# Performance work log

Measured on AMD Instinct MI355X. Metric: run time of the kernel, lower is better.

## Reference

```python
import jax, jax.numpy as jnp
import numpy as np

B, NV, CIN, C = 1, 40000, 128, 64
D, H, W = 19, 200, 176  # sparse_shape = output_shape[1:4] + [1,0,0]
EPS = 1e-3
DN = ('NCDHW', 'OIDHW', 'NCDHW')


def setup_inputs():
    key = jax.random.key(0)
    ks = jax.random.split(key, 12)
    vf = jax.random.normal(ks[0], (NV, CIN), jnp.float32)
    bi = jnp.zeros((NV, 1), jnp.int32)
    zi = jax.random.randint(ks[1], (NV, 1), 0, D, jnp.int32)
    yi = jax.random.randint(ks[2], (NV, 1), 0, H, jnp.int32)
    xi = jax.random.randint(ks[3], (NV, 1), 0, W, jnp.int32)
    coors = jnp.concatenate([bi, zi, yi, xi], axis=1)  # [batch, z, y, x]
    s = 0.05
    w_sub1 = jax.random.normal(ks[4], (C, CIN, 3, 3, 3), jnp.float32) * s
    w_down1 = jax.random.normal(ks[5], (C, C, 3, 1, 1), jnp.float32) * s
    w_sub2 = jax.random.normal(ks[6], (C, C, 3, 3, 3), jnp.float32) * s
    w_sub3 = jax.random.normal(ks[7], (C, C, 3, 3, 3), jnp.float32) * s
    w_down2 = jax.random.normal(ks[8], (C, C, 3, 1, 1), jnp.float32) * s
    bn_gamma = 1.0 + 0.1 * jax.random.normal(ks[9], (5, C), jnp.float32)
    bn_beta = 0.1 * jax.random.normal(ks[10], (5, C), jnp.float32)
    bn_mean = 0.1 * jax.random.normal(ks[11], (5, C), jnp.float32)
    bn_var = jnp.ones((5, C), jnp.float32)
    return dict(voxel_features=vf, coors=coors, batch_size=1,
                w_sub1=w_sub1, w_down1=w_down1, w_sub2=w_sub2, w_sub3=w_sub3,
                w_down2=w_down2, bn_gamma=bn_gamma, bn_beta=bn_beta,
                bn_mean=bn_mean, bn_var=bn_var)


def _conv(x, w, stride, pad):
    return jax.lax.conv_general_dilated(x, w, stride, pad, dimension_numbers=DN)


def _bnrelu(x, i, mask, g, b, m, v):
    # eval-mode BN on active sites only (inactive sites stay exactly zero -> mask)
    inv = jax.lax.rsqrt(v[i] + EPS)
    y = (x - m[i][None, :, None, None, None]) * (g[i] * inv)[None, :, None, None, None] \
        + b[i][None, :, None, None, None]
    return jnp.maximum(y, 0.0) * mask


def _forward(voxel_features, coors, batch_size, w_sub1, w_down1, w_sub2, w_sub3,
             w_down2, bn_gamma, bn_beta, bn_mean, bn_var):
    bi, zi, yi, xi = coors[:, 0], coors[:, 1], coors[:, 2], coors[:, 3]
    # scn.InputLayer: scatter (sum duplicates) active voxel features into dense grid
    dense = jnp.zeros((batch_size, D, H, W, CIN), voxel_features.dtype)
    dense = dense.at[bi, zi, yi, xi].add(voxel_features)
    x = jnp.transpose(dense, (0, 4, 1, 2, 3))  # NCDHW
    mask = jnp.zeros((batch_size, D, H, W), voxel_features.dtype)
    mask = mask.at[bi, zi, yi, xi].set(1.0)[:, None]  # [B,1,D,H,W] active sites
    ones_k = jnp.ones((1, 1, 3, 1, 1), x.dtype)
    pad1 = ((1, 1), (1, 1), (1, 1))
    bn = (bn_gamma, bn_beta, bn_mean, bn_var)
    # SubmanifoldConvolution(128->64, k3) + BNReLU : output only at active sites
    x = _bnrelu(_conv(x, w_sub1, (1, 1, 1), pad1) * mask, 0, mask, *bn)
    # Convolution 64->64 kernel (3,1,1) stride (2,1,1): new active set = any input in window
    x = _conv(x, w_down1, (2, 1, 1), 'VALID')
    mask = (_conv(mask, ones_k, (2, 1, 1), 'VALID') > 0).astype(x.dtype)
    x = _bnrelu(x, 1, mask, *bn)
    # two more submanifold convs
    x = _bnrelu(_conv(x, w_sub2, (1, 1, 1), pad1) * mask, 2, mask, *bn)
    x = _bnrelu(_conv(x, w_sub3, (1, 1, 1), pad1) * mask, 3, mask, *bn)
    # second strided conv
    x = _conv(x, w_down2, (2, 1, 1), 'VALID')
    mask = (_conv(mask, ones_k, (2, 1, 1), 'VALID') > 0).astype(x.dtype)
    x = _bnrelu(x, 4, mask, *bn)
    # SparseToDense then view(N, C*D, H, W)
    Nb, Cc, Dd, Hh, Ww = x.shape
    return x.reshape(Nb, Cc * Dd, Hh, Ww)


def reference(voxel_features, coors, batch_size, w_sub1, w_down1, w_sub2, w_sub3,
              w_down2, bn_gamma, bn_beta, bn_mean, bn_var):
    return _forward(voxel_features, coors, batch_size, w_sub1, w_down1, w_sub2,
                    w_sub3, w_down2, bn_gamma, bn_beta, bn_mean, bn_var)
```

## Files before the change

kernel.cpp:

```cpp
#include <hip/hip_runtime.h>

typedef float floatx4 __attribute__((ext_vector_type(4)));
typedef __bf16 bf16x8 __attribute__((ext_vector_type(8)));

#define D0_ 19
#define H0_ 200
#define W0_ 176
#define HW_ (H0_*W0_)
#define NCELL0 (D0_*HW_)
#define D1_ 9
#define NCELL1 (D1_*HW_)
#define D2_ 4
#define NCELL2 (D2_*HW_)
#define NV_ 40000
#define CAP0 40000
#define CAP1 80000
#define CAP2 140800
#define EPS_ 1e-3f

typedef __attribute__((address_space(1))) const unsigned int* gas_t;
typedef __attribute__((address_space(3))) unsigned int* las_t;

__device__ __forceinline__ float bf2f(short s){
    union { unsigned u; float f; } x; x.u = ((unsigned)(unsigned short)s) << 16; return x.f;
}
__device__ __forceinline__ short f2bf(float f){
    union { float f; unsigned u; } x; x.f = f;
    unsigned r = x.u + 0x7fffu + ((x.u >> 16) & 1u);
    return (short)(r >> 16);
}

__device__ __forceinline__ void repack_one(const float* w, short* Bout, int i, int KCsrc, int NSP){
    int k = i >> 6, n = i & 63;
    int ci = k & 127;
    int cis = (KCsrc == 128) ? ci : (ci & 63);
    short val = f2bf(w[(n * KCsrc + cis) * NSP + (k >> 7)]);
    int kc = k >> 5, lanehi = (k >> 3) & 3, jj = k & 7;
    int nt = n >> 4, lane = lanehi * 16 + (n & 15);
    Bout[((kc * 4 + nt) * 64 + lane) * 8 + jj] = val;
}

#define RP_BIG (3456*64)
#define RP_SML (384*64)

__global__ void k_prep(const float* w1, const float* w2, const float* w3,
                       const float* wd1, const float* wd2,
                       short* B1, short* B2, short* B3, short* Bd1, short* Bd2,
                       const float* g, const float* b, const float* m, const float* v,
                       float* scale, float* shift){
    int i = blockIdx.x * 256 + threadIdx.x;
    if (i < RP_BIG){ repack_one(w1, B1, i, 128, 27); return; }
    i -= RP_BIG;
    if (i < RP_BIG){ repack_one(w2, B2, i, 64, 27); return; }
    i -= RP_BIG;
    if (i < RP_BIG){ repack_one(w3, B3, i, 64, 27); return; }
    i -= RP_BIG;
    if (i < RP_SML){ repack_one(wd1, Bd1, i, 64, 3); return; }
    i -= RP_SML;
    if (i < RP_SML){ repack_one(wd2, Bd2, i, 64, 3); return; }
    i -= RP_SML;
    if (i < 5*64){
        float s = g[i] / sqrtf(v[i] + EPS_);
        scale[i] = s;
        shift[i] = b[i] - m[i] * s;
    }
}
#define PREP_TOT (3*RP_BIG + 2*RP_SML + 5*64)

__global__ void k_count(const int* coors, int* cntg){
    int v = blockIdx.x * 256 + threadIdx.x;
    if (v >= NV_) return;
    int z = coors[v*4+1], y = coors[v*4+2], x = coors[v*4+3];
    atomicAdd(&cntg[(z*H0_ + y)*W0_ + x], 1);
}

__device__ __forceinline__ int blk_rank(bool act, int* cnt, int& r_out){
    unsigned long long mask = __ballot(act);
    int lane = threadIdx.x & 63, wid = threadIdx.x >> 6;
    int wrank = __popcll(mask & ((1ull << lane) - 1));
    __shared__ int ws[4];
    __shared__ int blkbase;
    if (lane == 0) ws[wid] = __popcll(mask);
    __syncthreads();
    if (threadIdx.x == 0){
        int t0 = ws[0], t1 = ws[1], t2 = ws[2], t3 = ws[3];
        int tot = t0 + t1 + t2 + t3;
        blkbase = tot ? atomicAdd(cnt, tot) : 0;
        ws[0] = 0; ws[1] = t0; ws[2] = t0 + t1; ws[3] = t0 + t1 + t2;
    }
    __syncthreads();
    r_out = blkbase + ws[wid] + wrank;
    return 0;
}

__global__ void k_compact0(const int* cntg, int* idx0, int* list0, int* cnt0){
    int c = blockIdx.x * 256 + threadIdx.x;
    bool act = (c < NCELL0) && (cntg[c] > 0);
    int r; blk_rank(act, cnt0, r);
    if (c >= NCELL0) return;
    if (act){
        idx0[c] = r;
        int z = c / HW_; int rem = c - z * HW_;
        int y = rem / W0_; int x = rem - y * W0_;
        list0[r] = (z << 16) | (y << 8) | x;
    } else idx0[c] = -1;
}

__global__ void k_compact_dn(const int* idxsrc, int* idxdst, int* listdst, int* cnt,
                             int ncell){
    int c = blockIdx.x * 256 + threadIdx.x;
    bool act = false;
    int d = 0, y = 0, x = 0;
    if (c < ncell){
        d = c / HW_; int rem = c - d * HW_;
        y = rem / W0_; x = rem - y * W0_;
        #pragma unroll
        for (int j = 0; j < 3; ++j)
            act = act || (idxsrc[((2*d + j)*H0_ + y)*W0_ + x] >= 0);
    }
    int r; blk_rank(act, cnt, r);
    if (c >= ncell) return;
    if (act){
        idxdst[c] = r;
        listdst[r] = (d << 16) | (y << 8) | x;
    } else idxdst[c] = -1;
}

__global__ void k_scatter(const float* vf, const int* coors, const int* cntg,
                          const int* idx0, float* feat0f){
    int u = blockIdx.x * 256 + threadIdx.x;
    if (u >= NV_ * 32) return;
    int v = u >> 5, c4 = u & 31;
    int z = coors[v*4+1], y = coors[v*4+2], x = coors[v*4+3];
    int cell = (z*H0_ + y)*W0_ + x;
    int row = idx0[cell];
    float4 s = ((const float4*)(vf + (long)v * 128))[c4];
    float* dst = feat0f + (long)row * 128 + c4 * 4;
    if (cntg[cell] == 1){
        *(float4*)dst = s;
    } else {
        atomicAdd(dst+0, s.x); atomicAdd(dst+1, s.y);
        atomicAdd(dst+2, s.z); atomicAdd(dst+3, s.w);
    }
}

__global__ void k_convert(const float* f, short* b, const int* cntp){
    int n8 = cntp[0] * 16;
    int i = blockIdx.x * 256 + threadIdx.x;
    if (i >= n8) return;
    float4 a = ((const float4*)f)[i*2], c = ((const float4*)f)[i*2+1];
    short o[8] = { f2bf(a.x), f2bf(a.y), f2bf(a.z), f2bf(a.w),
                   f2bf(c.x), f2bf(c.y), f2bf(c.z), f2bf(c.w) };
    ((int4*)b)[i] = *(int4*)o;
}

__global__ void k_nbr27(const int* list0, const int* list1,
                        const int* idx0, const int* idx1,
                        int* nbr0T, int* nbr1T, const int* counters){
    int lvl = blockIdx.z;
    int j = blockIdx.y;
    int site = blockIdx.x * 256 + threadIdx.x;
    int M = counters[lvl];
    if (site >= M) return;
    const int* list = lvl ? list1 : list0;
    const int* idxg = lvl ? idx1 : idx0;
    int Dd = lvl ? D1_ : D0_;
    int cap = lvl ? CAP1 : CAP0;
    int cell = list[site];
    int z = cell >> 16, y = (cell >> 8) & 255, x = cell & 255;
    int nz = z + j/9 - 1, ny = y + (j/3)%3 - 1, nx = x + j%3 - 1;
    int r = -1;
    if ((unsigned)nz < (unsigned)Dd && (unsigned)ny < H0_ && (unsigned)nx < W0_)
        r = idxg[(nz*H0_ + ny)*W0_ + nx];
    (lvl ? nbr1T : nbr0T)[j * cap + site] = r;
}

__global__ void k_nbr3(const int* list1, const int* list2,
                       const int* idx0, const int* idx1,
                       int* dnb1T, int* dnb2T, const int* counters){
    int lvl = blockIdx.z;
    int j = blockIdx.y;
    int site = blockIdx.x * 256 + threadIdx.x;
    int M = counters[lvl + 1];
    if (site >= M) return;
    const int* list = lvl ? list2 : list1;
    const int* idxg = lvl ? idx1 : idx0;
    int cap = lvl ? CAP2 : CAP1;
    int cell = list[site];
    int d = cell >> 16, y = (cell >> 8) & 255, x = cell & 255;
    (lvl ? dnb2T : dnb1T)[j * cap + site] = idxg[((2*d + j)*H0_ + y)*W0_ + x];
}

template<int NNBR, bool FINAL>
__global__ __launch_bounds__(256) void k_gemm(
    const short* __restrict__ featA, const int* __restrict__ nbrT, int nstride,
    const short* __restrict__ Bs, short* __restrict__ out,
    const int* __restrict__ cntp,
    const float* __restrict__ scale, const float* __restrict__ shift,
    const int* __restrict__ list, float* __restrict__ dout)
{
    __shared__ short Blds[2][16*64*8];
    int M = *cntp;
    int m0 = blockIdx.x * 128;
    if (m0 >= M) return;
    int tid = threadIdx.x;
    int wave = tid >> 6, lane = tid & 63;
    int m16 = lane & 15;
    int koff = (lane >> 4) * 8;

    int row0 = m0 + wave * 16 + m16;
    int row1 = row0 + 64;
    bool ok0 = row0 < M, ok1 = row1 < M;

    floatx4 acc0[4] = {}, acc1[4] = {};
    bf16x8 A0[2][4], A1[2][4];
    const bf16x8 z8 = {0,0,0,0,0,0,0,0};

    auto stageB = [&](int j, int b){
        #pragma unroll
        for (int f = 0; f < 4; ++f){
            int frag = wave * 4 + f;
            const short* g = Bs + (((long)j * 16 + frag) * 64 + lane) * 8;
            __builtin_amdgcn_global_load_lds((gas_t)g, (las_t)&Blds[b][frag * 512],
                                             16, 0, 0);
        }
    };
    auto loadA1 = [&](bf16x8* dst, int r, int kc){
        dst[kc] = (r >= 0) ? *(const bf16x8*)(featA + (long)r*128 + koff + kc*32) : z8;
    };

    int rc0 = ok0 ? nbrT[row0] : -1;
    int rc1 = ok1 ? nbrT[row1] : -1;
    stageB(0, 0);
    #pragma unroll
    for (int kc = 0; kc < 4; ++kc){ loadA1(A0[0], rc0, kc); loadA1(A1[0], rc1, kc); }
    int rb0 = (NNBR > 1 && ok0) ? nbrT[nstride + row0] : -1;
    int rb1 = (NNBR > 1 && ok1) ? nbrT[nstride + row1] : -1;
    int ra0 = -1, ra1 = -1;
    __syncthreads();

    #pragma unroll
    for (int t = 0; t < NNBR; ++t){
        if (t + 1 < NNBR){
            stageB(t + 1, (t + 1) & 1);
            #pragma unroll
            for (int kc = 0; kc < 4; ++kc){ loadA1(A0[(t+1)&1], rb0, kc); loadA1(A1[(t+1)&1], rb1, kc); }
        }
        if (t + 2 < NNBR){
            ra0 = ok0 ? nbrT[(t+2)*nstride + row0] : -1;
            ra1 = ok1 ? nbrT[(t+2)*nstride + row1] : -1;
        }
        const short* Bb = Blds[t & 1];
        #pragma unroll
        for (int kc = 0; kc < 4; ++kc){
            bf16x8 b[4];
            #pragma unroll
            for (int nt = 0; nt < 4; ++nt)
                b[nt] = *(const bf16x8*)&Bb[((kc*4 + nt) * 64 + lane) * 8];
            bf16x8 a0 = A0[t&1][kc], a1 = A1[t&1][kc];
            #pragma unroll
            for (int nt = 0; nt < 4; ++nt)
                acc0[nt] = __builtin_amdgcn_mfma_f32_16x16x32_bf16(a0, b[nt], acc0[nt], 0, 0, 0);
            #pragma unroll
            for (int nt = 0; nt < 4; ++nt)
                acc1[nt] = __builtin_amdgcn_mfma_f32_16x16x32_bf16(a1, b[nt], acc1[nt], 0, 0, 0);
        }
        rb0 = ra0; rb1 = ra1;
        __syncthreads();
    }

    int n16 = lane & 15;
    #pragma unroll
    for (int rg = 0; rg < 2; ++rg){
        const floatx4* ac = rg ? acc1 : acc0;
        int mb = m0 + (wave + rg*4) * 16 + (lane >> 4) * 4;
        #pragma unroll
        for (int nt = 0; nt < 4; ++nt){
            int n = nt * 16 + n16;
            float sc = scale[n], sh = shift[n];
            #pragma unroll
            for (int r = 0; r < 4; ++r){
                int site = mb + r;
                if (site < M){
                    float y = fmaxf(ac[nt][r] * sc + sh, 0.f);
                    if (FINAL){
                        int cell = list[site];
                        int d = cell >> 16, yy = (cell >> 8) & 255, xx = cell & 255;
                        dout[((n*4 + d)*H0_ + yy)*W0_ + xx] = y;
                    } else {
                        short hi = f2bf(y);
                        float lo = y - bf2f(hi);
                        out[(long)site*128 + n]      = hi;
                        out[(long)site*128 + 64 + n] = f2bf(lo);
                    }
                }
            }
        }
    }
}

extern "C" void kernel_launch(void* const* d_in, const int* in_sizes, int n_in,
                              void* d_out, int out_size, void* d_ws, size_t ws_size,
                              hipStream_t stream){
    const float* vf   = (const float*)d_in[0];
    const int*   coors= (const int*)  d_in[1];
    const float* w1   = (const float*)d_in[3];
    const float* wd1  = (const float*)d_in[4];
    const float* w2   = (const float*)d_in[5];
    const float* w3   = (const float*)d_in[6];
    const float* wd2  = (const float*)d_in[7];
    const float* bng  = (const float*)d_in[8];
    const float* bnb  = (const float*)d_in[9];
    const float* bnm  = (const float*)d_in[10];
    const float* bnv  = (const float*)d_in[11];
    float* dout = (float*)d_out;

    char* ws = (char*)d_ws;
    size_t off = 0;
    auto alloc = [&](size_t bytes)->char* {
        char* p = ws + off;
        off += (bytes + 255) & ~(size_t)255;
        return p;
    };

    int*   counters = (int*)  alloc(256);
    int*   cntg     = (int*)  alloc((size_t)NCELL0 * 4);
    int*   idx0     = (int*)  alloc((size_t)NCELL0 * 4);
    int*   idx1     = (int*)  alloc((size_t)NCELL1 * 4);
    int*   idx2     = (int*)  alloc((size_t)NCELL2 * 4);
    int*   list0    = (int*)  alloc((size_t)CAP0 * 4);
    int*   list1    = (int*)  alloc((size_t)CAP1 * 4);
    int*   list2    = (int*)  alloc((size_t)CAP2 * 4);
    float* feat0f   = (float*)alloc((size_t)CAP0 * 128 * 4);
    short* feat0b   = (short*)alloc((size_t)CAP0 * 128 * 2);
    short* feat1    = (short*)alloc((size_t)CAP0 * 128 * 2);
    short* featd1   = (short*)alloc((size_t)CAP1 * 128 * 2);
    short* feat3    = (short*)alloc((size_t)CAP1 * 128 * 2);
    int*   nbr0T    = (int*)  alloc((size_t)CAP0 * 27 * 4);
    int*   nbr1T    = (int*)  alloc((size_t)CAP1 * 27 * 4);
    int*   dnb1T    = (int*)  alloc((size_t)CAP1 * 3 * 4);
    int*   dnb2T    = (int*)  alloc((size_t)CAP2 * 3 * 4);
    short* B1  = (short*)alloc((size_t)3456 * 64 * 2);
    short* B2  = (short*)alloc((size_t)3456 * 64 * 2);
    short* B3  = (short*)alloc((size_t)3456 * 64 * 2);
    short* Bd1 = (short*)alloc((size_t)384 * 64 * 2);
    short* Bd2 = (short*)alloc((size_t)384 * 64 * 2);
    float* bnscale = (float*)alloc(5 * 64 * 4);
    float* bnshift = (float*)alloc(5 * 64 * 4);
    short* feat2 = (short*)feat0f;

    hipMemsetAsync(counters, 0, 256 + (size_t)NCELL0 * 4, stream);
    hipMemsetAsync(feat0f, 0, (size_t)CAP0 * 128 * 4, stream);
    hipMemsetAsync(dout, 0, (size_t)out_size * 4, stream);

    k_prep<<<(PREP_TOT + 255)/256, 256, 0, stream>>>(w1, w2, w3, wd1, wd2,
        B1, B2, B3, Bd1, Bd2, bng, bnb, bnm, bnv, bnscale, bnshift);

    k_count<<<(NV_ + 255)/256, 256, 0, stream>>>(coors, cntg);
    k_compact0<<<(NCELL0 + 255)/256, 256, 0, stream>>>(cntg, idx0, list0, counters + 0);
    k_scatter<<<(NV_*32 + 255)/256, 256, 0, stream>>>(vf, coors, cntg, idx0, feat0f);
    k_convert<<<(CAP0*16 + 255)/256, 256, 0, stream>>>(feat0f, feat0b, counters + 0);
    k_compact_dn<<<(NCELL1 + 255)/256, 256, 0, stream>>>(idx0, idx1, list1, counters + 1, NCELL1);
    k_compact_dn<<<(NCELL2 + 255)/256, 256, 0, stream>>>(idx1, idx2, list2, counters + 2, NCELL2);

    dim3 g27((CAP1 + 255)/256, 27, 2);
    k_nbr27<<<g27, 256, 0, stream>>>(list0, list1, idx0, idx1, nbr0T, nbr1T, counters);
    dim3 g3((CAP2 + 255)/256, 3, 2);
    k_nbr3<<<g3, 256, 0, stream>>>(list1, list2, idx0, idx1, dnb1T, dnb2T, counters);

    k_gemm<27,false><<<(CAP0+127)/128, 256, 0, stream>>>(feat0b, nbr0T, CAP0, B1, feat1,
        counters + 0, bnscale + 0,   bnshift + 0,   nullptr, nullptr);
    k_gemm<3,false><<<(CAP1+127)/128, 256, 0, stream>>>(feat1, dnb1T, CAP1, Bd1, featd1,
        counters + 1, bnscale + 64,  bnshift + 64,  nullptr, nullptr);
    k_gemm<27,false><<<(CAP1+127)/128, 256, 0, stream>>>(featd1, nbr1T, CAP1, B2, feat2,
        counters + 1, bnscale + 128, bnshift + 128, nullptr, nullptr);
    k_gemm<27,false><<<(CAP1+127)/128, 256, 0, stream>>>(feat2, nbr1T, CAP1, B3, feat3,
        counters + 1, bnscale + 192, bnshift + 192, nullptr, nullptr);
    k_gemm<3,true><<<(CAP2+127)/128, 256, 0, stream>>>(feat3, dnb2T, CAP2, Bd2, nullptr,
        counters + 2, bnscale + 256, bnshift + 256, list2, dout);
}
```

Baseline: 354.8 us.

## Switch sparse conv GEMMs from split-bf16 to fp16 with halved K

Replaces bf16 storage with fp16 for features and weights. The hi/lo split-bf16 encoding, which doubled the channel dimension from 64 to 128 to keep precision, is dropped, so each intermediate layer stores 64 fp16 channels per row. The GEMM kernel gains an NCH template parameter, and later layers run half the K chunks and stage half the B tiles in shared memory. This cuts MFMA work and gather bandwidth for four of the five convolutions. It risks fp16 overflow and precision differences compared with the split representation.

```diff
diff --git a/kernel.cpp b/kernel.cpp
--- a/kernel.cpp
+++ b/kernel.cpp
@@ -1,7 +1,7 @@
 #include <hip/hip_runtime.h>
 
 typedef float floatx4 __attribute__((ext_vector_type(4)));
-typedef __bf16 bf16x8 __attribute__((ext_vector_type(8)));
+typedef _Float16 f16x8 __attribute__((ext_vector_type(8)));
 
 #define D0_ 19
 #define H0_ 200
@@ -21,27 +21,25 @@
 typedef __attribute__((address_space(1))) const unsigned int* gas_t;
 typedef __attribute__((address_space(3))) unsigned int* las_t;
 
-__device__ __forceinline__ float bf2f(short s){
-    union { unsigned u; float f; } x; x.u = ((unsigned)(unsigned short)s) << 16; return x.f;
-}
-__device__ __forceinline__ short f2bf(float f){
-    union { float f; unsigned u; } x; x.f = f;
-    unsigned r = x.u + 0x7fffu + ((x.u >> 16) & 1u);
-    return (short)(r >> 16);
-}
-
-__device__ __forceinline__ void repack_one(const float* w, short* Bout, int i, int KCsrc, int NSP){
+__device__ __forceinline__ short f2h(float f){
+    _Float16 h = (_Float16)f;
+    short s; __builtin_memcpy(&s, &h, 2); return s;
+}
+
+__device__ __forceinline__ void repack_one(const float* w, short* Bout, int i,
+                                           int KCsrc, int kshift, int NSP){
     int k = i >> 6, n = i & 63;
-    int ci = k & 127;
-    int cis = (KCsrc == 128) ? ci : (ci & 63);
-    short val = f2bf(w[(n * KCsrc + cis) * NSP + (k >> 7)]);
-    int kc = k >> 5, lanehi = (k >> 3) & 3, jj = k & 7;
+    int j = k >> kshift;
+    int ci = k & (KCsrc - 1);
+    short val = f2h(w[(n * KCsrc + ci) * NSP + j]);
+    int chunk = k >> 5, lanehi = (k >> 3) & 3, jj = k & 7;
     int nt = n >> 4, lane = lanehi * 16 + (n & 15);
-    Bout[((kc * 4 + nt) * 64 + lane) * 8 + jj] = val;
-}
-
-#define RP_BIG (3456*64)
-#define RP_SML (384*64)
+    Bout[((chunk * 4 + nt) * 64 + lane) * 8 + jj] = val;
+}
+
+#define RP1 (3456*64)
+#define RP2 (1728*64)
+#define RPD (192*64)
 
 __global__ void k_prep(const float* w1, const float* w2, const float* w3,
                        const float* wd1, const float* wd2,
@@ -49,23 +47,23 @@
                        const float* g, const float* b, const float* m, const float* v,
                        float* scale, float* shift){
     int i = blockIdx.x * 256 + threadIdx.x;
-    if (i < RP_BIG){ repack_one(w1, B1, i, 128, 27); return; }
-    i -= RP_BIG;
-    if (i < RP_BIG){ repack_one(w2, B2, i, 64, 27); return; }
-    i -= RP_BIG;
-    if (i < RP_BIG){ repack_one(w3, B3, i, 64, 27); return; }
-    i -= RP_BIG;
-    if (i < RP_SML){ repack_one(wd1, Bd1, i, 64, 3); return; }
-    i -= RP_SML;
-    if (i < RP_SML){ repack_one(wd2, Bd2, i, 64, 3); return; }
-    i -= RP_SML;
+    if (i < RP1){ repack_one(w1, B1, i, 128, 7, 27); return; }
+    i -= RP1;
+    if (i < RP2){ repack_one(w2, B2, i, 64, 6, 27); return; }
+    i -= RP2;
+    if (i < RP2){ repack_one(w3, B3, i, 64, 6, 27); return; }
+    i -= RP2;
+    if (i < RPD){ repack_one(wd1, Bd1, i, 64, 6, 3); return; }
+    i -= RPD;
+    if (i < RPD){ repack_one(wd2, Bd2, i, 64, 6, 3); return; }
+    i -= RPD;
     if (i < 5*64){
         float s = g[i] / sqrtf(v[i] + EPS_);
         scale[i] = s;
         shift[i] = b[i] - m[i] * s;
     }
 }
-#define PREP_TOT (3*RP_BIG + 2*RP_SML + 5*64)
+#define PREP_TOT (RP1 + 2*RP2 + 2*RPD + 5*64)
 
 __global__ void k_count(const int* coors, int* cntg){
     int v = blockIdx.x * 256 + threadIdx.x;
@@ -149,8 +147,8 @@
     int i = blockIdx.x * 256 + threadIdx.x;
     if (i >= n8) return;
     float4 a = ((const float4*)f)[i*2], c = ((const float4*)f)[i*2+1];
-    short o[8] = { f2bf(a.x), f2bf(a.y), f2bf(a.z), f2bf(a.w),
-                   f2bf(c.x), f2bf(c.y), f2bf(c.z), f2bf(c.w) };
+    short o[8] = { f2h(a.x), f2h(a.y), f2h(a.z), f2h(a.w),
+                   f2h(c.x), f2h(c.y), f2h(c.z), f2h(c.w) };
     ((int4*)b)[i] = *(int4*)o;
 }
 
@@ -191,7 +189,7 @@
     (lvl ? dnb2T : dnb1T)[j * cap + site] = idxg[((2*d + j)*H0_ + y)*W0_ + x];
 }
 
-template<int NNBR, bool FINAL>
+template<int NNBR, int NCH, bool FINAL>
 __global__ __launch_bounds__(256) void k_gemm(
     const short* __restrict__ featA, const int* __restrict__ nbrT, int nstride,
     const short* __restrict__ Bs, short* __restrict__ out,
@@ -199,7 +197,7 @@
     const float* __restrict__ scale, const float* __restrict__ shift,
     const int* __restrict__ list, float* __restrict__ dout)
 {
-    __shared__ short Blds[2][16*64*8];
+    __shared__ short Blds[2][NCH*4*512];
     int M = *cntp;
     int m0 = blockIdx.x * 128;
     if (m0 >= M) return;
@@ -207,33 +205,34 @@
     int wave = tid >> 6, lane = tid & 63;
     int m16 = lane & 15;
     int koff = (lane >> 4) * 8;
+    const int ROWS = NCH * 32;
 
     int row0 = m0 + wave * 16 + m16;
     int row1 = row0 + 64;
     bool ok0 = row0 < M, ok1 = row1 < M;
 
     floatx4 acc0[4] = {}, acc1[4] = {};
-    bf16x8 A0[2][4], A1[2][4];
-    const bf16x8 z8 = {0,0,0,0,0,0,0,0};
+    f16x8 A0[2][NCH], A1[2][NCH];
+    const f16x8 z8 = {0,0,0,0,0,0,0,0};
 
     auto stageB = [&](int j, int b){
         #pragma unroll
-        for (int f = 0; f < 4; ++f){
-            int frag = wave * 4 + f;
-            const short* g = Bs + (((long)j * 16 + frag) * 64 + lane) * 8;
+        for (int f = 0; f < NCH; ++f){
+            int frag = wave * NCH + f;
+            const short* g = Bs + (((long)j * NCH * 4 + frag) * 64 + lane) * 8;
             __builtin_amdgcn_global_load_lds((gas_t)g, (las_t)&Blds[b][frag * 512],
                                              16, 0, 0);
         }
     };
-    auto loadA1 = [&](bf16x8* dst, int r, int kc){
-        dst[kc] = (r >= 0) ? *(const bf16x8*)(featA + (long)r*128 + koff + kc*32) : z8;
+    auto loadA1 = [&](f16x8* dst, int r, int kc){
+        dst[kc] = (r >= 0) ? *(const f16x8*)(featA + (long)r*ROWS + koff + kc*32) : z8;
     };
 
     int rc0 = ok0 ? nbrT[row0] : -1;
     int rc1 = ok1 ? nbrT[row1] : -1;
     stageB(0, 0);
     #pragma unroll
-    for (int kc = 0; kc < 4; ++kc){ loadA1(A0[0], rc0, kc); loadA1(A1[0], rc1, kc); }
+    for (int kc = 0; kc < NCH; ++kc){ loadA1(A0[0], rc0, kc); loadA1(A1[0], rc1, kc); }
     int rb0 = (NNBR > 1 && ok0) ? nbrT[nstride + row0] : -1;
     int rb1 = (NNBR > 1 && ok1) ? nbrT[nstride + row1] : -1;
     int ra0 = -1, ra1 = -1;
@@ -244,7 +243,7 @@
         if (t + 1 < NNBR){
             stageB(t + 1, (t + 1) & 1);
             #pragma unroll
-            for (int kc = 0; kc < 4; ++kc){ loadA1(A0[(t+1)&1], rb0, kc); loadA1(A1[(t+1)&1], rb1, kc); }
+            for (int kc = 0; kc < NCH; ++kc){ loadA1(A0[(t+1)&1], rb0, kc); loadA1(A1[(t+1)&1], rb1, kc); }
         }
         if (t + 2 < NNBR){
             ra0 = ok0 ? nbrT[(t+2)*nstride + row0] : -1;
@@ -252,18 +251,18 @@
         }
         const short* Bb = Blds[t & 1];
         #pragma unroll
-        for (int kc = 0; kc < 4; ++kc){
-            bf16x8 b[4];
+        for (int kc = 0; kc < NCH; ++kc){
+            f16x8 b[4];
             #pragma unroll
             for (int nt = 0; nt < 4; ++nt)
-                b[nt] = *(const bf16x8*)&Bb[((kc*4 + nt) * 64 + lane) * 8];
-            bf16x8 a0 = A0[t&1][kc], a1 = A1[t&1][kc];
+                b[nt] = *(const f16x8*)&Bb[((kc*4 + nt) * 64 + lane) * 8];
+            f16x8 a0 = A0[t&1][kc], a1 = A1[t&1][kc];
             #pragma unroll
             for (int nt = 0; nt < 4; ++nt)
-                acc0[nt] = __builtin_amdgcn_mfma_f32_16x16x32_bf16(a0, b[nt], acc0[nt], 0, 0, 0);
+                acc0[nt] = __builtin_amdgcn_mfma_f32_16x16x32_f16(a0, b[nt], acc0[nt], 0, 0, 0);
             #pragma unroll
             for (int nt = 0; nt < 4; ++nt)
-                acc1[nt] = __builtin_amdgcn_mfma_f32_16x16x32_bf16(a1, b[nt], acc1[nt], 0, 0, 0);
+                acc1[nt] = __builtin_amdgcn_mfma_f32_16x16x32_f16(a1, b[nt], acc1[nt], 0, 0, 0);
         }
         rb0 = ra0; rb1 = ra1;
         __syncthreads();
@@ -288,10 +287,7 @@
                         int d = cell >> 16, yy = (cell >> 8) & 255, xx = cell & 255;
                         dout[((n*4 + d)*H0_ + yy)*W0_ + xx] = y;
                     } else {
-                        short hi = f2bf(y);
-                        float lo = y - bf2f(hi);
-                        out[(long)site*128 + n]      = hi;
-                        out[(long)site*128 + 64 + n] = f2bf(lo);
+                        out[(long)site*64 + n] = f2h(y);
                     }
                 }
             }
@@ -332,22 +328,22 @@
     int*   list1    = (int*)  alloc((size_t)CAP1 * 4);
     int*   list2    = (int*)  alloc((size_t)CAP2 * 4);
     float* feat0f   = (float*)alloc((size_t)CAP0 * 128 * 4);
-    short* feat0b   = (short*)alloc((size_t)CAP0 * 128 * 2);
-    short* feat1    = (short*)alloc((size_t)CAP0 * 128 * 2);
-    short* featd1   = (short*)alloc((size_t)CAP1 * 128 * 2);
-    short* feat3    = (short*)alloc((size_t)CAP1 * 128 * 2);
+    short* feat0h   = (short*)alloc((size_t)CAP0 * 128 * 2);
+    short* feat1    = (short*)alloc((size_t)CAP0 * 64 * 2);
+    short* featd1   = (short*)alloc((size_t)CAP1 * 64 * 2);
+    short* feat2    = (short*)alloc((size_t)CAP1 * 64 * 2);
+    short* feat3    = (short*)alloc((size_t)CAP1 * 64 * 2);
     int*   nbr0T    = (int*)  alloc((size_t)CAP0 * 27 * 4);
     int*   nbr1T    = (int*)  alloc((size_t)CAP1 * 27 * 4);
     int*   dnb1T    = (int*)  alloc((size_t)CAP1 * 3 * 4);
     int*   dnb2T    = (int*)  alloc((size_t)CAP2 * 3 * 4);
     short* B1  = (short*)alloc((size_t)3456 * 64 * 2);
-    short* B2  = (short*)alloc((size_t)3456 * 64 * 2);
-    short* B3  = (short*)alloc((size_t)3456 * 64 * 2);
-    short* Bd1 = (short*)alloc((size_t)384 * 64 * 2);
-    short* Bd2 = (short*)alloc((size_t)384 * 64 * 2);
+    short* B2  = (short*)alloc((size_t)1728 * 64 * 2);
+    short* B3  = (short*)alloc((size_t)1728 * 64 * 2);
+    short* Bd1 = (short*)alloc((size_t)192 * 64 * 2);
+    short* Bd2 = (short*)alloc((size_t)192 * 64 * 2);
     float* bnscale = (float*)alloc(5 * 64 * 4);
     float* bnshift = (float*)alloc(5 * 64 * 4);
-    short* feat2 = (short*)feat0f;
 
     hipMemsetAsync(counters, 0, 256 + (size_t)NCELL0 * 4, stream);
     hipMemsetAsync(feat0f, 0, (size_t)CAP0 * 128 * 4, stream);
@@ -359,7 +355,7 @@
     k_count<<<(NV_ + 255)/256, 256, 0, stream>>>(coors, cntg);
     k_compact0<<<(NCELL0 + 255)/256, 256, 0, stream>>>(cntg, idx0, list0, counters + 0);
     k_scatter<<<(NV_*32 + 255)/256, 256, 0, stream>>>(vf, coors, cntg, idx0, feat0f);
-    k_convert<<<(CAP0*16 + 255)/256, 256, 0, stream>>>(feat0f, feat0b, counters + 0);
+    k_convert<<<(CAP0*16 + 255)/256, 256, 0, stream>>>(feat0f, feat0h, counters + 0);
     k_compact_dn<<<(NCELL1 + 255)/256, 256, 0, stream>>>(idx0, idx1, list1, counters + 1, NCELL1);
     k_compact_dn<<<(NCELL2 + 255)/256, 256, 0, stream>>>(idx1, idx2, list2, counters + 2, NCELL2);
 
@@ -368,14 +364,14 @@
     dim3 g3((CAP2 + 255)/256, 3, 2);
     k_nbr3<<<g3, 256, 0, stream>>>(list1, list2, idx0, idx1, dnb1T, dnb2T, counters);
 
-    k_gemm<27,false><<<(CAP0+127)/128, 256, 0, stream>>>(feat0b, nbr0T, CAP0, B1, feat1,
+    k_gemm<27,4,false><<<(CAP0+127)/128, 256, 0, stream>>>(feat0h, nbr0T, CAP0, B1, feat1,
         counters + 0, bnscale + 0,   bnshift + 0,   nullptr, nullptr);
-    k_gemm<3,false><<<(CAP1+127)/128, 256, 0, stream>>>(feat1, dnb1T, CAP1, Bd1, featd1,
+    k_gemm<3,2,false><<<(CAP1+127)/128, 256, 0, stream>>>(feat1, dnb1T, CAP1, Bd1, featd1,
         counters + 1, bnscale + 64,  bnshift + 64,  nullptr, nullptr);
-    k_gemm<27,false><<<(CAP1+127)/128, 256, 0, stream>>>(featd1, nbr1T, CAP1, B2, feat2,
+    k_gemm<27,2,false><<<(CAP1+127)/128, 256, 0, stream>>>(featd1, nbr1T, CAP1, B2, feat2,
         counters + 1, bnscale + 128, bnshift + 128, nullptr, nullptr);
-    k_gemm<27,false><<<(CAP1+127)/128, 256, 0, stream>>>(feat2, nbr1T, CAP1, B3, feat3,
+    k_gemm<27,2,false><<<(CAP1+127)/128, 256, 0, stream>>>(feat2, nbr1T, CAP1, B3, feat3,
         counters + 1, bnscale + 192, bnshift + 192, nullptr, nullptr);
-    k_gemm<3,true><<<(CAP2+127)/128, 256, 0, stream>>>(feat3, dnb2T, CAP2, Bd2, nullptr,
+    k_gemm<3,2,true><<<(CAP2+127)/128, 256, 0, stream>>>(feat3, dnb2T, CAP2, Bd2, nullptr,
         counters + 2, bnscale + 256, bnshift + 256, list2, dout);
 }
```

Result: faster. 322.1 us (-9.2%).
